# Performance work log

Hardware: AMD Instinct MI355X
Metric: run time of the kernel (lower is better)

## Reference

```python
import jax, jax.numpy as jnp
import numpy as np

N_NODES = 50000
N_EDGES = 600000
DIM = 128
K = 3
N_LAYERS = 3
LEAKY_SLOPE = 0.01  # nn.LeakyReLU default
RE_NORM = 1.0       # 2/lambda_max with lambda_max=2 (standard ChebNet approximation)


def setup_inputs() -> dict:
    key = jax.random.key(0)
    ks = jax.random.split(key, 8)
    weights = jax.random.normal(ks[0], (N_NODES,), dtype=jnp.float32)
    src = jax.random.randint(ks[1], (N_EDGES,), 0, N_NODES)
    dst = jax.random.randint(ks[2], (N_EDGES,), 0, N_NODES)
    lin_in_w = jax.random.normal(ks[3], (1, DIM), dtype=jnp.float32) * 0.5
    lin_in_b = jnp.zeros((DIM,), dtype=jnp.float32)
    cheb_ws = jax.random.normal(ks[4], (N_LAYERS, K * DIM, DIM), dtype=jnp.float32) * 0.05
    cheb_bs = jnp.zeros((N_LAYERS, DIM), dtype=jnp.float32)
    pred_w = jax.random.normal(ks[5], (DIM, 1), dtype=jnp.float32) * 0.05
    pred_b = jnp.zeros((1,), dtype=jnp.float32)
    return {"weights": weights, "src": src, "dst": dst,
            "lin_in_w": lin_in_w, "lin_in_b": lin_in_b,
            "cheb_ws": cheb_ws, "cheb_bs": cheb_bs,
            "pred_w": pred_w, "pred_b": pred_b}


def _cheb_conv(x, W, b, src, dst, d_invsqrt, n):
    # DGL ChebConv with lambda_max=2 -> re_norm=1: scaled Laplacian L_hat = -D^-1/2 A D^-1/2
    def spmm(f):  # unnormalized Laplacian-style aggregation: D^-1/2 A D^-1/2 f
        h = f * d_invsqrt
        agg = jax.ops.segment_sum(h[src], dst, num_segments=n)
        return agg * d_invsqrt

    X0 = x
    terms = [X0]
    h = spmm(X0)
    X1 = -RE_NORM * h + X0 * (RE_NORM - 1.0)
    terms.append(X1)
    for _ in range(2, K):
        h = spmm(X1)
        Xi = -2.0 * RE_NORM * h + X1 * (2.0 * (RE_NORM - 1.0)) - X0
        terms.append(Xi)
        X0, X1 = X1, Xi
    Xt = jnp.concatenate(terms, axis=1)  # [N, K*DIM]
    return jax.nn.relu(Xt @ W + b)       # DGL ChebConv default activation=F.relu


def reference(weights, src, dst, lin_in_w, lin_in_b, cheb_ws, cheb_bs, pred_w, pred_b):
    n = weights.shape[0]
    # dgl.add_self_loop
    loop = jnp.arange(n, dtype=src.dtype)
    src_f = jnp.concatenate([src, loop])
    dst_f = jnp.concatenate([dst, loop])
    # in-degree normalization D^-1/2 (clamp min 1)
    deg = jax.ops.segment_sum(jnp.ones_like(dst_f, dtype=jnp.float32), dst_f, num_segments=n)
    d_invsqrt = jnp.power(jnp.clip(deg, 1.0), -0.5)[:, None]  # [N,1]

    feat = weights[:, None] @ lin_in_w + lin_in_b             # [N, DIM]
    emb = _cheb_conv(feat, cheb_ws[0], cheb_bs[0], src_f, dst_f, d_invsqrt, n)
    for i in range(1, N_LAYERS):
        emb = jax.nn.leaky_relu(emb, negative_slope=LEAKY_SLOPE)
        emb = _cheb_conv(emb, cheb_ws[i], cheb_bs[i], src_f, dst_f, d_invsqrt, n)
    logits = emb @ pred_w + pred_b                            # do_train=True path
    return logits
```

## Files before the change

kernel.cpp:

```cpp
#include <hip/hip_runtime.h>

typedef unsigned int uint;
typedef unsigned short ushort;

#define NN 50000
#define NE 600000
#define DIM 128
#define KD 384
#define PADK 40

typedef __attribute__((ext_vector_type(8))) short short8;
typedef __attribute__((ext_vector_type(4))) float float4v;

static __device__ __forceinline__ ushort f2b(float f) {
    uint u = __float_as_uint(f);
    return (ushort)((u + 0x7FFFu + ((u >> 16) & 1u)) >> 16);
}
static __device__ __forceinline__ float blo(uint u) { return __uint_as_float(u << 16); }
static __device__ __forceinline__ float bhi(uint u) { return __uint_as_float(u & 0xFFFF0000u); }

__global__ void k_init(int* __restrict__ cnt, const float* __restrict__ cw,
                       ushort* __restrict__ wt, const float* __restrict__ lw,
                       const float* __restrict__ lb, float* __restrict__ uvout) {
    if (blockIdx.x < 49) {
        int i = blockIdx.x * 256 + threadIdx.x;
        if (i < 12544) ((int4*)cnt)[i] = make_int4(0, 0, 0, 0);
    } else if (blockIdx.x < 625) {
        int i = (blockIdx.x - 49) * 256 + threadIdx.x;
        if (i < 3 * KD * DIM) {
            int l = i / (KD * DIM), rem = i - l * (KD * DIM);
            int k = rem >> 7, n = rem & 127;
            wt[(size_t)l * KD * DIM + (size_t)n * KD + k] = f2b(cw[i]);
        }
    } else {
        int vec = blockIdx.x - 625;
        int t = vec >> 1;
        const float* coef = (vec & 1) ? lb : lw;
        int c = threadIdx.x;
        if (c < 128) {
            float s = 0.f;
#pragma unroll 8
            for (int k = 0; k < 128; ++k)
                s = fmaf(coef[k], cw[(size_t)(t * 128 + k) * 128 + c], s);
            uvout[vec * 128 + c] = s;
        }
    }
}

__global__ void k_hist(const int* __restrict__ dst, int* __restrict__ cnt) {
    int e = blockIdx.x * 256 + threadIdx.x;
    if (e < NE) atomicAdd(&cnt[dst[e]], 1);
}

__global__ __launch_bounds__(256) void k_scan1(const int* __restrict__ cnt,
                                               int* __restrict__ incl,
                                               int* __restrict__ bsums,
                                               float* __restrict__ dinv) {
    __shared__ int sh[256];
    int i = blockIdx.x * 256 + threadIdx.x;
    int v = (i < NN) ? cnt[i] : 0;
    if (i < NN) dinv[i] = rsqrtf((float)(v + 1));
    sh[threadIdx.x] = v;
    __syncthreads();
    for (int d = 1; d < 256; d <<= 1) {
        int t = (threadIdx.x >= d) ? sh[threadIdx.x - d] : 0;
        __syncthreads();
        sh[threadIdx.x] += t;
        __syncthreads();
    }
    incl[i] = sh[threadIdx.x];
    if (threadIdx.x == 255) bsums[blockIdx.x] = sh[255];
}

__global__ __launch_bounds__(256) void k_scan3(const int* __restrict__ cnt,
                                               int* __restrict__ incl_cursor,
                                               const int* __restrict__ bsums,
                                               int* __restrict__ offs) {
    __shared__ int sh[256];
    __shared__ int boff;
    int tid = threadIdx.x;
    int v = (tid < 196) ? bsums[tid] : 0;
    sh[tid] = v;
    __syncthreads();
    for (int d = 1; d < 256; d <<= 1) {
        int t = (tid >= d) ? sh[tid - d] : 0;
        __syncthreads();
        sh[tid] += t;
        __syncthreads();
    }
    if (tid == blockIdx.x) boff = sh[tid] - v;
    __syncthreads();
    int i = blockIdx.x * 256 + tid;
    if (i >= NN) return;
    int excl = incl_cursor[i] - cnt[i] + boff;
    offs[i] = excl;
    incl_cursor[i] = excl;
    if (i == NN - 1) offs[NN] = NE;
}

__global__ void k_fill(const int* __restrict__ src, const int* __restrict__ dst,
                       int* __restrict__ cursor, const float* __restrict__ dinv,
                       const float* __restrict__ w_in,
                       uint2* __restrict__ csrE, float* __restrict__ hw) {
    int e = blockIdx.x * 256 + threadIdx.x;
    if (e < NE) {
        int s = src[e], d = dst[e];
        int p = atomicAdd(&cursor[d], 1);
        float ds = dinv[s];
        uint2 rec;
        rec.x = (uint)s;
        rec.y = __float_as_uint(ds * dinv[d]);
        csrE[p] = rec;
        hw[p] = ds * w_in[s];
    }
}

__global__ __launch_bounds__(256) void k_spmv1(
        const int* __restrict__ offs, const uint2* __restrict__ csrE,
        const float* __restrict__ hw, const float* __restrict__ dinv,
        const float* __restrict__ w, float2* __restrict__ SS) {
    int n = blockIdx.x * 16 + (threadIdx.x >> 4);
    int l = threadIdx.x & 15;
    int j0 = offs[n], j1 = offs[n + 1];
    float sA = 0.f, sB = 0.f;
    const float* ew = (const float*)csrE;
    for (int j = j0 + l; j < j1; j += 16) {
        sA += hw[j];
        sB += ew[2 * j + 1];
    }
#pragma unroll
    for (int off = 8; off > 0; off >>= 1) {
        sA += __shfl_down(sA, off, 16);
        sB += __shfl_down(sB, off, 16);
    }
    if (l == 0) {
        float dn = dinv[n], id = dn * dn;
        float2 o;
        o.x = dn * sA + id * w[n];
        o.y = sB + id;
        SS[n] = o;
    }
}

__global__ __launch_bounds__(256) void k_spmv2l1(
        const int* __restrict__ offs, const uint2* __restrict__ csrE,
        const float2* __restrict__ SS, const float* __restrict__ dinv,
        const float* __restrict__ w, const float* __restrict__ uv,
        const float* __restrict__ bias, ushort* __restrict__ Pb) {
    __shared__ float suv[768];
    __shared__ float sbias[128];
    int tid = threadIdx.x;
    for (int i = tid; i < 768; i += 256) suv[i] = uv[i];
    if (tid < 128) sbias[tid] = bias[tid];
    __syncthreads();

    int n = blockIdx.x * 16 + (tid >> 4);
    int l = tid & 15;
    int j0 = offs[n], j1 = offs[n + 1];
    float sC = 0.f, sD = 0.f;
    for (int j = j0 + l; j < j1; j += 16) {
        uint2 e = csrE[j];
        float wv = __uint_as_float(e.y);
        float2 s = SS[e.x];
        sC = fmaf(wv, s.x, sC);
        sD = fmaf(wv, s.y, sD);
    }
#pragma unroll
    for (int off = 8; off > 0; off >>= 1) {
        sC += __shfl_down(sC, off, 16);
        sD += __shfl_down(sD, off, 16);
    }
    sC = __shfl(sC, 0, 16);
    sD = __shfl(sD, 0, 16);

    float dn = dinv[n], id = dn * dn;
    float2 s = SS[n];
    float ssw = sC + id * s.x;
    float ss1 = sD + id * s.y;
    float a0 = w[n];
    float a1 = -s.x, b1 = -s.y;
    float a2 = 2.f * ssw - a0, b2 = 2.f * ss1 - 1.f;

    const float2* uv2 = (const float2*)suv;
    uint r[4];
#pragma unroll
    for (int q = 0; q < 4; ++q) {
        int p = 4 * l + q;
        float2 u0 = uv2[p],       v0 = uv2[64 + p];
        float2 u1 = uv2[128 + p], v1 = uv2[192 + p];
        float2 u2 = uv2[256 + p], v2 = uv2[320 + p];
        float2 bb = ((const float2*)sbias)[p];
        float o0 = bb.x + a0 * u0.x + v0.x + a1 * u1.x + b1 * v1.x + a2 * u2.x + b2 * v2.x;
        float o1 = bb.y + a0 * u0.y + v0.y + a1 * u1.y + b1 * v1.y + a2 * u2.y + b2 * v2.y;
        r[q] = (uint)f2b(fmaxf(o0, 0.f)) | ((uint)f2b(fmaxf(o1, 0.f)) << 16);
    }
    uint4 w4; w4.x = r[0]; w4.y = r[1]; w4.z = r[2]; w4.w = r[3];
    ((uint4*)(Pb + (size_t)n * DIM))[l] = w4;
}

__global__ __launch_bounds__(256) void k_gather1(
        const ushort* __restrict__ Xb, const int* __restrict__ offs,
        const uint2* __restrict__ csrE, const float* __restrict__ dinv,
        ushort* __restrict__ Qb) {
    int n = __builtin_amdgcn_readfirstlane(blockIdx.x * 4 + (threadIdx.x >> 6));
    int lane = threadIdx.x & 63;
    int j0 = offs[n], j1 = offs[n + 1];
    const uint* Xu = (const uint*)Xb;
    float a0 = 0.f, a1 = 0.f;
#pragma unroll 4
    for (int j = j0; j < j1; ++j) {
        uint2 e = csrE[j];
        float wv = __uint_as_float(e.y);
        uint u = Xu[(size_t)e.x * 64 + lane];
        a0 = fmaf(wv, blo(u), a0);
        a1 = fmaf(wv, bhi(u), a1);
    }
    float dn = dinv[n];
    float id = dn * dn;
    uint un = Xu[(size_t)n * 64 + lane];
    uint ow = (uint)f2b(-(a0 + blo(un) * id))
            | ((uint)f2b(-(a1 + bhi(un) * id)) << 16);
    ((uint*)Qb)[(size_t)n * 64 + lane] = ow;
}

__global__ __launch_bounds__(256) void k_gather2(
        const ushort* __restrict__ X1b, const ushort* __restrict__ X0b,
        const int* __restrict__ offs, const uint2* __restrict__ csrE,
        const float* __restrict__ dinv, ushort* __restrict__ Rb) {
    int n = __builtin_amdgcn_readfirstlane(blockIdx.x * 4 + (threadIdx.x >> 6));
    int lane = threadIdx.x & 63;
    int j0 = offs[n], j1 = offs[n + 1];
    const uint* Xu = (const uint*)X1b;
    float a0 = 0.f, a1 = 0.f;
#pragma unroll 4
    for (int j = j0; j < j1; ++j) {
        uint2 e = csrE[j];
        float wv = __uint_as_float(e.y);
        uint u = Xu[(size_t)e.x * 64 + lane];
        a0 = fmaf(wv, blo(u), a0);
        a1 = fmaf(wv, bhi(u), a1);
    }
    float dn = dinv[n];
    float id = dn * dn;
    uint u1n = Xu[(size_t)n * 64 + lane];
    uint u0n = ((const uint*)X0b)[(size_t)n * 64 + lane];
    uint ow = (uint)f2b(-2.f * (a0 + blo(u1n) * id) - blo(u0n))
            | ((uint)f2b(-2.f * (a1 + bhi(u1n) * id) - bhi(u0n)) << 16);
    ((uint*)Rb)[(size_t)n * 64 + lane] = ow;
}

__global__ __launch_bounds__(256) void k_gemm(
        const ushort* __restrict__ X0b, const ushort* __restrict__ X1b,
        const ushort* __restrict__ X2b, const ushort* __restrict__ Wt,
        const float* __restrict__ bias, ushort* __restrict__ outb) {
    __shared__ ushort As[128 * PADK];
    __shared__ ushort Bs[128 * PADK];
    int tid = threadIdx.x;
    int nbase = blockIdx.x * 128;
    int wave = tid >> 6, lane = tid & 63;
    int wr = wave >> 1, wc = wave & 1;
    int l15 = lane & 15, quad = lane >> 4;

    float4v acc[4][4];
#pragma unroll
    for (int i = 0; i < 4; ++i)
#pragma unroll
        for (int j = 0; j < 4; ++j) acc[i][j] = (float4v)0.f;

    int srow = tid >> 1, shalf = tid & 1;
    int gm = nbase + srow; if (gm >= NN) gm = NN - 1;

    for (int c = 0; c < 12; ++c) {
        int part = c >> 2;
        int k0 = (c & 3) * 32;
        const ushort* Xp = (part == 0) ? X0b : ((part == 1) ? X1b : X2b);
        const uint4* ga = (const uint4*)(Xp + (size_t)gm * DIM + k0 + shalf * 16);
        uint4 a0 = ga[0], a1 = ga[1];
        const uint4* gb = (const uint4*)(Wt + (size_t)srow * KD + c * 32 + shalf * 16);
        uint4 b0 = gb[0], b1 = gb[1];
        __syncthreads();
        uint4* pa = (uint4*)(As + srow * PADK + shalf * 16);
        pa[0] = a0; pa[1] = a1;
        uint4* pb = (uint4*)(Bs + srow * PADK + shalf * 16);
        pb[0] = b0; pb[1] = b1;
        __syncthreads();
        short8 af[4], bf[4];
#pragma unroll
        for (int i = 0; i < 4; ++i) {
            af[i] = *(const short8*)(As + (wr * 64 + i * 16 + l15) * PADK + quad * 8);
            bf[i] = *(const short8*)(Bs + (wc * 64 + i * 16 + l15) * PADK + quad * 8);
        }
#pragma unroll
        for (int i = 0; i < 4; ++i)
#pragma unroll
            for (int j = 0; j < 4; ++j)
                acc[i][j] = __builtin_amdgcn_mfma_f32_16x16x32_bf16(
                    af[i], bf[j], acc[i][j], 0, 0, 0);
    }

    float bv[4];
#pragma unroll
    for (int j = 0; j < 4; ++j) bv[j] = bias[wc * 64 + j * 16 + l15];
#pragma unroll
    for (int i = 0; i < 4; ++i) {
#pragma unroll
        for (int r = 0; r < 4; ++r) {
            int node = nbase + wr * 64 + i * 16 + quad * 4 + r;
            if (node < NN) {
#pragma unroll
                for (int j = 0; j < 4; ++j) {
                    int col = wc * 64 + j * 16 + l15;
                    outb[(size_t)node * DIM + col] =
                        f2b(fmaxf(acc[i][j][r] + bv[j], 0.f));
                }
            }
        }
    }
}

__global__ __launch_bounds__(256) void k_gemm_pred(
        const ushort* __restrict__ X0b, const ushort* __restrict__ X1b,
        const ushort* __restrict__ X2b, const ushort* __restrict__ Wt,
        const float* __restrict__ bias, const float* __restrict__ pw,
        const float* __restrict__ pb, float* __restrict__ logits) {
    __shared__ ushort As[128 * PADK];
    __shared__ ushort Bs[128 * PADK];
    __shared__ float lsum[128];
    int tid = threadIdx.x;
    int nbase = blockIdx.x * 128;
    int wave = tid >> 6, lane = tid & 63;
    int wr = wave >> 1, wc = wave & 1;
    int l15 = lane & 15, quad = lane >> 4;

    float4v acc[4][4];
#pragma unroll
    for (int i = 0; i < 4; ++i)
#pragma unroll
        for (int j = 0; j < 4; ++j) acc[i][j] = (float4v)0.f;

    int srow = tid >> 1, shalf = tid & 1;
    int gm = nbase + srow; if (gm >= NN) gm = NN - 1;

    for (int c = 0; c < 12; ++c) {
        int part = c >> 2;
        int k0 = (c & 3) * 32;
        const ushort* Xp = (part == 0) ? X0b : ((part == 1) ? X1b : X2b);
        const uint4* ga = (const uint4*)(Xp + (size_t)gm * DIM + k0 + shalf * 16);
        uint4 a0 = ga[0], a1 = ga[1];
        const uint4* gb = (const uint4*)(Wt + (size_t)srow * KD + c * 32 + shalf * 16);
        uint4 b0 = gb[0], b1 = gb[1];
        __syncthreads();
        uint4* pa = (uint4*)(As + srow * PADK + shalf * 16);
        pa[0] = a0; pa[1] = a1;
        uint4* pb2 = (uint4*)(Bs + srow * PADK + shalf * 16);
        pb2[0] = b0; pb2[1] = b1;
        __syncthreads();
        short8 af[4], bf[4];
#pragma unroll
        for (int i = 0; i < 4; ++i) {
            af[i] = *(const short8*)(As + (wr * 64 + i * 16 + l15) * PADK + quad * 8);
            bf[i] = *(const short8*)(Bs + (wc * 64 + i * 16 + l15) * PADK + quad * 8);
        }
#pragma unroll
        for (int i = 0; i < 4; ++i)
#pragma unroll
            for (int j = 0; j < 4; ++j)
                acc[i][j] = __builtin_amdgcn_mfma_f32_16x16x32_bf16(
                    af[i], bf[j], acc[i][j], 0, 0, 0);
    }

    __syncthreads();
    if (tid < 128) lsum[tid] = 0.f;
    __syncthreads();
    float bv[4], pwv[4];
#pragma unroll
    for (int j = 0; j < 4; ++j) {
        int col = wc * 64 + j * 16 + l15;
        bv[j] = bias[col];
        pwv[j] = pw[col];
    }
#pragma unroll
    for (int i = 0; i < 4; ++i) {
#pragma unroll
        for (int r = 0; r < 4; ++r) {
            float local = 0.f;
#pragma unroll
            for (int j = 0; j < 4; ++j)
                local = fmaf(fmaxf(acc[i][j][r] + bv[j], 0.f), pwv[j], local);
            local += __shfl_xor(local, 1, 64);
            local += __shfl_xor(local, 2, 64);
            local += __shfl_xor(local, 4, 64);
            local += __shfl_xor(local, 8, 64);
            if (l15 == 0)
                atomicAdd(&lsum[wr * 64 + i * 16 + quad * 4 + r], local);
        }
    }
    __syncthreads();
    if (tid < 128) {
        int node = nbase + tid;
        if (node < NN) logits[node] = lsum[tid] + pb[0];
    }
}

extern "C" void kernel_launch(void* const* d_in, const int* in_sizes, int n_in,
                              void* d_out, int out_size, void* d_ws, size_t ws_size,
                              hipStream_t stream) {
    int i_weights = 0, i_src = 1, i_dst = 2, i_lw = 3, i_lb = 4,
        i_cw = 5, i_cb = 6, i_pw = 7, i_pb = 8;
    {
        int seen600k = 0, seen128 = 0;
        for (int i = 0; i < n_in; ++i) {
            int s = in_sizes[i];
            if (s == 50000) i_weights = i;
            else if (s == 600000) { if (seen600k == 0) i_src = i; else i_dst = i; ++seen600k; }
            else if (s == 128) { if (seen128 == 0) i_lw = i; else if (seen128 == 1) i_lb = i; else i_pw = i; ++seen128; }
            else if (s == 147456) i_cw = i;
            else if (s == 384) i_cb = i;
            else if (s == 1) i_pb = i;
        }
    }
    const float* weights = (const float*)d_in[i_weights];
    const int*   src     = (const int*)d_in[i_src];
    const int*   dst     = (const int*)d_in[i_dst];
    const float* lin_w   = (const float*)d_in[i_lw];
    const float* lin_b   = (const float*)d_in[i_lb];
    const float* cheb_w  = (const float*)d_in[i_cw];
    const float* cheb_b  = (const float*)d_in[i_cb];
    const float* pred_w  = (const float*)d_in[i_pw];
    const float* pred_b  = (const float*)d_in[i_pb];
    float* out = (float*)d_out;

    float*  ws      = (float*)d_ws;
    float*  dinv    = ws;
    int*    offs    = (int*)(ws + 50048);
    int*    cnt     = offs + 50056;
    int*    incl    = cnt + 50176;
    int*    bsums   = incl + 50176;
    uint2*  csrE    = (uint2*)(bsums + 256);
    float*  hw      = (float*)(csrE + NE);
    float2* SS      = (float2*)(hw + NE);
    float*  uv      = (float*)(SS + 50048);
    ushort* Pb      = (ushort*)(uv + 768);
    ushort* Qb      = Pb + (size_t)NN * DIM;
    ushort* Rb      = Qb + (size_t)NN * DIM;
    ushort* Wtb     = Rb + (size_t)NN * DIM;

    k_init<<<631, 256, 0, stream>>>(cnt, cheb_w, Wtb, lin_w, lin_b, uv);
    k_hist<<<2344, 256, 0, stream>>>(dst, cnt);
    k_scan1<<<196, 256, 0, stream>>>(cnt, incl, bsums, dinv);
    k_scan3<<<196, 256, 0, stream>>>(cnt, incl, bsums, offs);
    k_fill<<<2344, 256, 0, stream>>>(src, dst, incl, dinv, weights, csrE, hw);

    k_spmv1<<<3125, 256, 0, stream>>>(offs, csrE, hw, dinv, weights, SS);
    k_spmv2l1<<<3125, 256, 0, stream>>>(offs, csrE, SS, dinv, weights, uv,
                                        cheb_b, Pb);

    k_gather1<<<12500, 256, 0, stream>>>(Pb, offs, csrE, dinv, Qb);
    k_gather2<<<12500, 256, 0, stream>>>(Qb, Pb, offs, csrE, dinv, Rb);
    k_gemm<<<391, 256, 0, stream>>>(Pb, Qb, Rb, Wtb + (size_t)KD * DIM,
                                    cheb_b + DIM, Pb);
    k_gather1<<<12500, 256, 0, stream>>>(Pb, offs, csrE, dinv, Qb);
    k_gather2<<<12500, 256, 0, stream>>>(Qb, Pb, offs, csrE, dinv, Rb);
    k_gemm_pred<<<391, 256, 0, stream>>>(Pb, Qb, Rb, Wtb + (size_t)2 * KD * DIM,
                                         cheb_b + 2 * DIM, pred_w, pred_b, out);
}
```

Baseline: 323.3 us.

## Split feature matrices into four 32-column chunks for cache-local gathers

Stores the bf16 node feature matrices as four separate column chunks of 32 values, each a contiguous array over all nodes, instead of one row-major 128-wide layout. Gather kernels now assign a 16-lane group per node per chunk and loop over nodes with a fixed grid, so each gather pass works on a 3.2MB chunk that fits in cache better. The GEMM kernels and the layer-1 producer are adapted to read and write the chunked layout. The trade-off is that each edge's CSR entry is read four times (once per chunk) and each gather is 64 bytes instead of 256 bytes.

```diff
diff --git a/kernel.cpp b/kernel.cpp
--- a/kernel.cpp
+++ b/kernel.cpp
@@ -8,6 +8,7 @@
 #define DIM 128
 #define KD 384
 #define PADK 40
+#define CHS ((size_t)NN * 32)
 
 typedef __attribute__((ext_vector_type(8))) short short8;
 typedef __attribute__((ext_vector_type(4))) float float4v;
@@ -195,58 +196,67 @@
         r[q] = (uint)f2b(fmaxf(o0, 0.f)) | ((uint)f2b(fmaxf(o1, 0.f)) << 16);
     }
     uint4 w4; w4.x = r[0]; w4.y = r[1]; w4.z = r[2]; w4.w = r[3];
-    ((uint4*)(Pb + (size_t)n * DIM))[l] = w4;
-}
-
-__global__ __launch_bounds__(256) void k_gather1(
-        const ushort* __restrict__ Xb, const int* __restrict__ offs,
+    *(uint4*)(Pb + (size_t)(l >> 2) * CHS + (size_t)n * 32 + (l & 3) * 8) = w4;
+}
+
+__global__ __launch_bounds__(256, 8) void k_gather1x(
+        const ushort* __restrict__ Xc, const int* __restrict__ offs,
         const uint2* __restrict__ csrE, const float* __restrict__ dinv,
-        ushort* __restrict__ Qb) {
-    int n = __builtin_amdgcn_readfirstlane(blockIdx.x * 4 + (threadIdx.x >> 6));
-    int lane = threadIdx.x & 63;
-    int j0 = offs[n], j1 = offs[n + 1];
-    const uint* Xu = (const uint*)Xb;
-    float a0 = 0.f, a1 = 0.f;
+        ushort* __restrict__ Qc) {
+    int chunk = blockIdx.x & 3;
+    int grp = threadIdx.x >> 4;
+    int d = threadIdx.x & 15;
+    const uint* Xu = (const uint*)(Xc + (size_t)chunk * CHS);
+    uint* Qu = (uint*)(Qc + (size_t)chunk * CHS);
+    int g0 = ((blockIdx.x >> 2) << 4) + grp;
+    for (int n = g0; n < NN; n += 8192) {
+        int j0 = offs[n], j1 = offs[n + 1];
+        float a0 = 0.f, a1 = 0.f;
 #pragma unroll 4
-    for (int j = j0; j < j1; ++j) {
-        uint2 e = csrE[j];
-        float wv = __uint_as_float(e.y);
-        uint u = Xu[(size_t)e.x * 64 + lane];
-        a0 = fmaf(wv, blo(u), a0);
-        a1 = fmaf(wv, bhi(u), a1);
-    }
-    float dn = dinv[n];
-    float id = dn * dn;
-    uint un = Xu[(size_t)n * 64 + lane];
-    uint ow = (uint)f2b(-(a0 + blo(un) * id))
-            | ((uint)f2b(-(a1 + bhi(un) * id)) << 16);
-    ((uint*)Qb)[(size_t)n * 64 + lane] = ow;
-}
-
-__global__ __launch_bounds__(256) void k_gather2(
-        const ushort* __restrict__ X1b, const ushort* __restrict__ X0b,
+        for (int j = j0; j < j1; ++j) {
+            uint2 e = csrE[j];
+            float wv = __uint_as_float(e.y);
+            uint u = Xu[(size_t)e.x * 16 + d];
+            a0 = fmaf(wv, blo(u), a0);
+            a1 = fmaf(wv, bhi(u), a1);
+        }
+        float dn = dinv[n], id = dn * dn;
+        uint un = Xu[(size_t)n * 16 + d];
+        uint ow = (uint)f2b(-(a0 + blo(un) * id))
+                | ((uint)f2b(-(a1 + bhi(un) * id)) << 16);
+        Qu[(size_t)n * 16 + d] = ow;
+    }
+}
+
+__global__ __launch_bounds__(256, 8) void k_gather2x(
+        const ushort* __restrict__ X1c, const ushort* __restrict__ X0c,
         const int* __restrict__ offs, const uint2* __restrict__ csrE,
-        const float* __restrict__ dinv, ushort* __restrict__ Rb) {
-    int n = __builtin_amdgcn_readfirstlane(blockIdx.x * 4 + (threadIdx.x >> 6));
-    int lane = threadIdx.x & 63;
-    int j0 = offs[n], j1 = offs[n + 1];
-    const uint* Xu = (const uint*)X1b;
-    float a0 = 0.f, a1 = 0.f;
+        const float* __restrict__ dinv, ushort* __restrict__ Rc) {
+    int chunk = blockIdx.x & 3;
+    int grp = threadIdx.x >> 4;
+    int d = threadIdx.x & 15;
+    const uint* Xu = (const uint*)(X1c + (size_t)chunk * CHS);
+    const uint* X0u = (const uint*)(X0c + (size_t)chunk * CHS);
+    uint* Ru = (uint*)(Rc + (size_t)chunk * CHS);
+    int g0 = ((blockIdx.x >> 2) << 4) + grp;
+    for (int n = g0; n < NN; n += 8192) {
+        int j0 = offs[n], j1 = offs[n + 1];
+        float a0 = 0.f, a1 = 0.f;
 #pragma unroll 4
-    for (int j = j0; j < j1; ++j) {
-        uint2 e = csrE[j];
-        float wv = __uint_as_float(e.y);
-        uint u = Xu[(size_t)e.x * 64 + lane];
-        a0 = fmaf(wv, blo(u), a0);
-        a1 = fmaf(wv, bhi(u), a1);
-    }
-    float dn = dinv[n];
-    float id = dn * dn;
-    uint u1n = Xu[(size_t)n * 64 + lane];
-    uint u0n = ((const uint*)X0b)[(size_t)n * 64 + lane];
-    uint ow = (uint)f2b(-2.f * (a0 + blo(u1n) * id) - blo(u0n))
-            | ((uint)f2b(-2.f * (a1 + bhi(u1n) * id) - bhi(u0n)) << 16);
-    ((uint*)Rb)[(size_t)n * 64 + lane] = ow;
+        for (int j = j0; j < j1; ++j) {
+            uint2 e = csrE[j];
+            float wv = __uint_as_float(e.y);
+            uint u = Xu[(size_t)e.x * 16 + d];
+            a0 = fmaf(wv, blo(u), a0);
+            a1 = fmaf(wv, bhi(u), a1);
+        }
+        float dn = dinv[n], id = dn * dn;
+        uint u1n = Xu[(size_t)n * 16 + d];
+        uint u0n = X0u[(size_t)n * 16 + d];
+        uint ow = (uint)f2b(-2.f * (a0 + blo(u1n) * id) - blo(u0n))
+                | ((uint)f2b(-2.f * (a1 + bhi(u1n) * id) - bhi(u0n)) << 16);
+        Ru[(size_t)n * 16 + d] = ow;
+    }
 }
 
 __global__ __launch_bounds__(256) void k_gemm(
@@ -272,9 +282,10 @@
 
     for (int c = 0; c < 12; ++c) {
         int part = c >> 2;
-        int k0 = (c & 3) * 32;
+        int cki = c & 3;
         const ushort* Xp = (part == 0) ? X0b : ((part == 1) ? X1b : X2b);
-        const uint4* ga = (const uint4*)(Xp + (size_t)gm * DIM + k0 + shalf * 16);
+        const uint4* ga = (const uint4*)(Xp + (size_t)cki * CHS
+                                         + (size_t)gm * 32 + shalf * 16);
         uint4 a0 = ga[0], a1 = ga[1];
         const uint4* gb = (const uint4*)(Wt + (size_t)srow * KD + c * 32 + shalf * 16);
         uint4 b0 = gb[0], b1 = gb[1];
@@ -309,8 +320,8 @@
             if (node < NN) {
 #pragma unroll
                 for (int j = 0; j < 4; ++j) {
-                    int col = wc * 64 + j * 16 + l15;
-                    outb[(size_t)node * DIM + col] =
+                    outb[(size_t)(wc * 2 + (j >> 1)) * CHS + (size_t)node * 32
+                         + (j & 1) * 16 + l15] =
                         f2b(fmaxf(acc[i][j][r] + bv[j], 0.f));
                 }
             }
@@ -343,9 +354,10 @@
 
     for (int c = 0; c < 12; ++c) {
         int part = c >> 2;
-        int k0 = (c & 3) * 32;
+        int cki = c & 3;
         const ushort* Xp = (part == 0) ? X0b : ((part == 1) ? X1b : X2b);
-        const uint4* ga = (const uint4*)(Xp + (size_t)gm * DIM + k0 + shalf * 16);
+        const uint4* ga = (const uint4*)(Xp + (size_t)cki * CHS
+                                         + (size_t)gm * 32 + shalf * 16);
         uint4 a0 = ga[0], a1 = ga[1];
         const uint4* gb = (const uint4*)(Wt + (size_t)srow * KD + c * 32 + shalf * 16);
         uint4 b0 = gb[0], b1 = gb[1];
@@ -455,12 +467,12 @@
     k_spmv2l1<<<3125, 256, 0, stream>>>(offs, csrE, SS, dinv, weights, uv,
                                         cheb_b, Pb);
 
-    k_gather1<<<12500, 256, 0, stream>>>(Pb, offs, csrE, dinv, Qb);
-    k_gather2<<<12500, 256, 0, stream>>>(Qb, Pb, offs, csrE, dinv, Rb);
+    k_gather1x<<<2048, 256, 0, stream>>>(Pb, offs, csrE, dinv, Qb);
+    k_gather2x<<<2048, 256, 0, stream>>>(Qb, Pb, offs, csrE, dinv, Rb);
     k_gemm<<<391, 256, 0, stream>>>(Pb, Qb, Rb, Wtb + (size_t)KD * DIM,
                                     cheb_b + DIM, Pb);
-    k_gather1<<<12500, 256, 0, stream>>>(Pb, offs, csrE, dinv, Qb);
-    k_gather2<<<12500, 256, 0, stream>>>(Qb, Pb, offs, csrE, dinv, Rb);
+    k_gather1x<<<2048, 256, 0, stream>>>(Pb, offs, csrE, dinv, Qb);
+    k_gather2x<<<2048, 256, 0, stream>>>(Qb, Pb, offs, csrE, dinv, Rb);
     k_gemm_pred<<<391, 256, 0, stream>>>(Pb, Qb, Rb, Wtb + (size_t)2 * KD * DIM,
                                          cheb_b + 2 * DIM, pred_w, pred_b, out);
 }
```

Result: slower. 344.4 us (+6.5%).

## Record edge ranks in histogram and pack per-node and per-edge data into uint4 records

Applied to the files above, without the earlier changes.

The histogram pass now stores each edge's atomic rank, so the CSR fill computes its slot as offset plus rank and no longer needs a second atomic cursor pass. Per-node dinv, input weight and offset are packed into one uint4 record, and each CSR edge record (src, norm weight, scaled input) becomes a single uint4 instead of separate arrays. The gather kernels hoist their self-row loads ahead of the edge loop and unroll it by 8. In exchange, edge records are twice as wide, which raises edge-stream traffic in the gathers, and the separate rank array uses extra workspace.

```diff
diff --git a/kernel.cpp b/kernel.cpp
--- a/kernel.cpp
+++ b/kernel.cpp
@@ -18,6 +18,7 @@
 }
 static __device__ __forceinline__ float blo(uint u) { return __uint_as_float(u << 16); }
 static __device__ __forceinline__ float bhi(uint u) { return __uint_as_float(u & 0xFFFF0000u); }
+static __device__ __forceinline__ float asf(uint u) { return __uint_as_float(u); }
 
 __global__ void k_init(int* __restrict__ cnt, const float* __restrict__ cw,
                        ushort* __restrict__ wt, const float* __restrict__ lw,
@@ -47,19 +48,26 @@
     }
 }
 
-__global__ void k_hist(const int* __restrict__ dst, int* __restrict__ cnt) {
+__global__ void k_hist(const int* __restrict__ dst, int* __restrict__ cnt,
+                       int* __restrict__ rank) {
     int e = blockIdx.x * 256 + threadIdx.x;
-    if (e < NE) atomicAdd(&cnt[dst[e]], 1);
+    if (e < NE) rank[e] = atomicAdd(&cnt[dst[e]], 1);
 }
 
 __global__ __launch_bounds__(256) void k_scan1(const int* __restrict__ cnt,
                                                int* __restrict__ incl,
                                                int* __restrict__ bsums,
-                                               float* __restrict__ dinv) {
+                                               const float* __restrict__ w,
+                                               uint4* __restrict__ nrec) {
     __shared__ int sh[256];
     int i = blockIdx.x * 256 + threadIdx.x;
     int v = (i < NN) ? cnt[i] : 0;
-    if (i < NN) dinv[i] = rsqrtf((float)(v + 1));
+    if (i < NN) {
+        uint2 r;
+        r.x = __float_as_uint(rsqrtf((float)(v + 1)));
+        r.y = __float_as_uint(w[i]);
+        ((uint2*)nrec)[2 * i] = r;
+    }
     sh[threadIdx.x] = v;
     __syncthreads();
     for (int d = 1; d < 256; d <<= 1) {
@@ -73,9 +81,10 @@
 }
 
 __global__ __launch_bounds__(256) void k_scan3(const int* __restrict__ cnt,
-                                               int* __restrict__ incl_cursor,
+                                               const int* __restrict__ incl,
                                                const int* __restrict__ bsums,
-                                               int* __restrict__ offs) {
+                                               int* __restrict__ offs,
+                                               uint4* __restrict__ nrec) {
     __shared__ int sh[256];
     __shared__ int boff;
     int tid = threadIdx.x;
@@ -92,41 +101,43 @@
     __syncthreads();
     int i = blockIdx.x * 256 + tid;
     if (i >= NN) return;
-    int excl = incl_cursor[i] - cnt[i] + boff;
+    int excl = incl[i] - cnt[i] + boff;
     offs[i] = excl;
-    incl_cursor[i] = excl;
+    ((uint*)nrec)[4 * i + 2] = (uint)excl;
     if (i == NN - 1) offs[NN] = NE;
 }
 
 __global__ void k_fill(const int* __restrict__ src, const int* __restrict__ dst,
-                       int* __restrict__ cursor, const float* __restrict__ dinv,
-                       const float* __restrict__ w_in,
-                       uint2* __restrict__ csrE, float* __restrict__ hw) {
+                       const int* __restrict__ rank,
+                       const uint4* __restrict__ nrec,
+                       uint4* __restrict__ csrE2) {
     int e = blockIdx.x * 256 + threadIdx.x;
     if (e < NE) {
         int s = src[e], d = dst[e];
-        int p = atomicAdd(&cursor[d], 1);
-        float ds = dinv[s];
-        uint2 rec;
+        uint4 rs = nrec[s];
+        uint4 rd = nrec[d];
+        float ds = asf(rs.x), wsv = asf(rs.y), dd = asf(rd.x);
+        int p = (int)rd.z + rank[e];
+        uint4 rec;
         rec.x = (uint)s;
-        rec.y = __float_as_uint(ds * dinv[d]);
-        csrE[p] = rec;
-        hw[p] = ds * w_in[s];
+        rec.y = __float_as_uint(ds * dd);
+        rec.z = __float_as_uint(ds * wsv);
+        rec.w = 0;
+        csrE2[p] = rec;
     }
 }
 
 __global__ __launch_bounds__(256) void k_spmv1(
-        const int* __restrict__ offs, const uint2* __restrict__ csrE,
-        const float* __restrict__ hw, const float* __restrict__ dinv,
-        const float* __restrict__ w, float2* __restrict__ SS) {
+        const int* __restrict__ offs, const uint4* __restrict__ csrE2,
+        const uint4* __restrict__ nrec, float2* __restrict__ SS) {
     int n = blockIdx.x * 16 + (threadIdx.x >> 4);
     int l = threadIdx.x & 15;
     int j0 = offs[n], j1 = offs[n + 1];
     float sA = 0.f, sB = 0.f;
-    const float* ew = (const float*)csrE;
     for (int j = j0 + l; j < j1; j += 16) {
-        sA += hw[j];
-        sB += ew[2 * j + 1];
+        uint4 q = csrE2[j];
+        sA += asf(q.z);
+        sB += asf(q.y);
     }
 #pragma unroll
     for (int off = 8; off > 0; off >>= 1) {
@@ -134,19 +145,20 @@
         sB += __shfl_down(sB, off, 16);
     }
     if (l == 0) {
-        float dn = dinv[n], id = dn * dn;
+        uint4 nr = nrec[n];
+        float dn = asf(nr.x), id = dn * dn;
         float2 o;
-        o.x = dn * sA + id * w[n];
+        o.x = dn * sA + id * asf(nr.y);
         o.y = sB + id;
         SS[n] = o;
     }
 }
 
 __global__ __launch_bounds__(256) void k_spmv2l1(
-        const int* __restrict__ offs, const uint2* __restrict__ csrE,
-        const float2* __restrict__ SS, const float* __restrict__ dinv,
-        const float* __restrict__ w, const float* __restrict__ uv,
-        const float* __restrict__ bias, ushort* __restrict__ Pb) {
+        const int* __restrict__ offs, const uint4* __restrict__ csrE2,
+        const float2* __restrict__ SS, const uint4* __restrict__ nrec,
+        const float* __restrict__ uv, const float* __restrict__ bias,
+        ushort* __restrict__ Pb) {
     __shared__ float suv[768];
     __shared__ float sbias[128];
     int tid = threadIdx.x;
@@ -159,9 +171,9 @@
     int j0 = offs[n], j1 = offs[n + 1];
     float sC = 0.f, sD = 0.f;
     for (int j = j0 + l; j < j1; j += 16) {
-        uint2 e = csrE[j];
-        float wv = __uint_as_float(e.y);
-        float2 s = SS[e.x];
+        uint4 q = csrE2[j];
+        float wv = asf(q.y);
+        float2 s = SS[q.x];
         sC = fmaf(wv, s.x, sC);
         sD = fmaf(wv, s.y, sD);
     }
@@ -173,11 +185,12 @@
     sC = __shfl(sC, 0, 16);
     sD = __shfl(sD, 0, 16);
 
-    float dn = dinv[n], id = dn * dn;
+    uint4 nr = nrec[n];
+    float dn = asf(nr.x), id = dn * dn;
     float2 s = SS[n];
     float ssw = sC + id * s.x;
     float ss1 = sD + id * s.y;
-    float a0 = w[n];
+    float a0 = asf(nr.y);
     float a1 = -s.x, b1 = -s.y;
     float a2 = 2.f * ssw - a0, b2 = 2.f * ss1 - 1.f;
 
@@ -200,24 +213,24 @@
 
 __global__ __launch_bounds__(256) void k_gather1(
         const ushort* __restrict__ Xb, const int* __restrict__ offs,
-        const uint2* __restrict__ csrE, const float* __restrict__ dinv,
+        const uint4* __restrict__ csrE2, const uint4* __restrict__ nrec,
         ushort* __restrict__ Qb) {
     int n = __builtin_amdgcn_readfirstlane(blockIdx.x * 4 + (threadIdx.x >> 6));
     int lane = threadIdx.x & 63;
     int j0 = offs[n], j1 = offs[n + 1];
     const uint* Xu = (const uint*)Xb;
+    uint un = Xu[(size_t)n * 64 + lane];
+    float dn = asf(nrec[n].x);
     float a0 = 0.f, a1 = 0.f;
-#pragma unroll 4
+#pragma unroll 8
     for (int j = j0; j < j1; ++j) {
-        uint2 e = csrE[j];
-        float wv = __uint_as_float(e.y);
+        uint4 e = csrE2[j];
+        float wv = asf(e.y);
         uint u = Xu[(size_t)e.x * 64 + lane];
         a0 = fmaf(wv, blo(u), a0);
         a1 = fmaf(wv, bhi(u), a1);
     }
-    float dn = dinv[n];
     float id = dn * dn;
-    uint un = Xu[(size_t)n * 64 + lane];
     uint ow = (uint)f2b(-(a0 + blo(un) * id))
             | ((uint)f2b(-(a1 + bhi(un) * id)) << 16);
     ((uint*)Qb)[(size_t)n * 64 + lane] = ow;
@@ -225,25 +238,25 @@
 
 __global__ __launch_bounds__(256) void k_gather2(
         const ushort* __restrict__ X1b, const ushort* __restrict__ X0b,
-        const int* __restrict__ offs, const uint2* __restrict__ csrE,
-        const float* __restrict__ dinv, ushort* __restrict__ Rb) {
+        const int* __restrict__ offs, const uint4* __restrict__ csrE2,
+        const uint4* __restrict__ nrec, ushort* __restrict__ Rb) {
     int n = __builtin_amdgcn_readfirstlane(blockIdx.x * 4 + (threadIdx.x >> 6));
     int lane = threadIdx.x & 63;
     int j0 = offs[n], j1 = offs[n + 1];
     const uint* Xu = (const uint*)X1b;
+    uint u1n = Xu[(size_t)n * 64 + lane];
+    uint u0n = ((const uint*)X0b)[(size_t)n * 64 + lane];
+    float dn = asf(nrec[n].x);
     float a0 = 0.f, a1 = 0.f;
-#pragma unroll 4
+#pragma unroll 8
     for (int j = j0; j < j1; ++j) {
-        uint2 e = csrE[j];
-        float wv = __uint_as_float(e.y);
+        uint4 e = csrE2[j];
+        float wv = asf(e.y);
         uint u = Xu[(size_t)e.x * 64 + lane];
         a0 = fmaf(wv, blo(u), a0);
         a1 = fmaf(wv, bhi(u), a1);
     }
-    float dn = dinv[n];
     float id = dn * dn;
-    uint u1n = Xu[(size_t)n * 64 + lane];
-    uint u0n = ((const uint*)X0b)[(size_t)n * 64 + lane];
     uint ow = (uint)f2b(-2.f * (a0 + blo(u1n) * id) - blo(u0n))
             | ((uint)f2b(-2.f * (a1 + bhi(u1n) * id) - bhi(u0n)) << 16);
     ((uint*)Rb)[(size_t)n * 64 + lane] = ow;
@@ -430,37 +443,35 @@
     const float* pred_b  = (const float*)d_in[i_pb];
     float* out = (float*)d_out;
 
-    float*  ws      = (float*)d_ws;
-    float*  dinv    = ws;
-    int*    offs    = (int*)(ws + 50048);
+    uint4*  csrE2   = (uint4*)d_ws;
+    uint4*  nrec    = csrE2 + NE;
+    float2* SS      = (float2*)(nrec + 50048);
+    float*  uv      = (float*)(SS + 50048);
+    int*    offs    = (int*)(uv + 768);
     int*    cnt     = offs + 50056;
     int*    incl    = cnt + 50176;
     int*    bsums   = incl + 50176;
-    uint2*  csrE    = (uint2*)(bsums + 256);
-    float*  hw      = (float*)(csrE + NE);
-    float2* SS      = (float2*)(hw + NE);
-    float*  uv      = (float*)(SS + 50048);
-    ushort* Pb      = (ushort*)(uv + 768);
+    int*    rank    = bsums + 256;
+    ushort* Pb      = (ushort*)(rank + NE);
     ushort* Qb      = Pb + (size_t)NN * DIM;
     ushort* Rb      = Qb + (size_t)NN * DIM;
     ushort* Wtb     = Rb + (size_t)NN * DIM;
 
     k_init<<<631, 256, 0, stream>>>(cnt, cheb_w, Wtb, lin_w, lin_b, uv);
-    k_hist<<<2344, 256, 0, stream>>>(dst, cnt);
-    k_scan1<<<196, 256, 0, stream>>>(cnt, incl, bsums, dinv);
-    k_scan3<<<196, 256, 0, stream>>>(cnt, incl, bsums, offs);
-    k_fill<<<2344, 256, 0, stream>>>(src, dst, incl, dinv, weights, csrE, hw);
-
-    k_spmv1<<<3125, 256, 0, stream>>>(offs, csrE, hw, dinv, weights, SS);
-    k_spmv2l1<<<3125, 256, 0, stream>>>(offs, csrE, SS, dinv, weights, uv,
-                                        cheb_b, Pb);
-
-    k_gather1<<<12500, 256, 0, stream>>>(Pb, offs, csrE, dinv, Qb);
-    k_gather2<<<12500, 256, 0, stream>>>(Qb, Pb, offs, csrE, dinv, Rb);
+    k_hist<<<2344, 256, 0, stream>>>(dst, cnt, rank);
+    k_scan1<<<196, 256, 0, stream>>>(cnt, incl, bsums, weights, nrec);
+    k_scan3<<<196, 256, 0, stream>>>(cnt, incl, bsums, offs, nrec);
+    k_fill<<<2344, 256, 0, stream>>>(src, dst, rank, nrec, csrE2);
+
+    k_spmv1<<<3125, 256, 0, stream>>>(offs, csrE2, nrec, SS);
+    k_spmv2l1<<<3125, 256, 0, stream>>>(offs, csrE2, SS, nrec, uv, cheb_b, Pb);
+
+    k_gather1<<<12500, 256, 0, stream>>>(Pb, offs, csrE2, nrec, Qb);
+    k_gather2<<<12500, 256, 0, stream>>>(Qb, Pb, offs, csrE2, nrec, Rb);
     k_gemm<<<391, 256, 0, stream>>>(Pb, Qb, Rb, Wtb + (size_t)KD * DIM,
                                     cheb_b + DIM, Pb);
-    k_gather1<<<12500, 256, 0, stream>>>(Pb, offs, csrE, dinv, Qb);
-    k_gather2<<<12500, 256, 0, stream>>>(Qb, Pb, offs, csrE, dinv, Rb);
+    k_gather1<<<12500, 256, 0, stream>>>(Pb, offs, csrE2, nrec, Qb);
+    k_gather2<<<12500, 256, 0, stream>>>(Qb, Pb, offs, csrE2, nrec, Rb);
     k_gemm_pred<<<391, 256, 0, stream>>>(Pb, Qb, Rb, Wtb + (size_t)2 * KD * DIM,
                                          cheb_b + 2 * DIM, pred_w, pred_b, out);
 }
```

Result: faster. 308.3 us (-4.6%).
